# Kernel optimization log

Measured on AMD Instinct MI355X. Metric: run time of the kernel, lower is better.

## Reference

```python
import jax, jax.numpy as jnp
import numpy as np

K = 7  # kernel_size


def setup_inputs() -> dict:
    key = jax.random.key(0)
    k1, k2 = jax.random.split(key)
    kernels = jax.random.normal(k1, (4, K, K, 256, 256), dtype=jnp.float32)
    features = jax.random.normal(k2, (4, 96, 256, 256), dtype=jnp.float32)
    return {"kernels": kernels, "features": features}


def reference(kernels, features):
    # kernels: [b, k, k, h, w]; features: [b, c, h, w]
    # Equivalent to unfold(features) viewed as [b,c,k,k,h,w] contracted with
    # kernels via einsum 'bcklhw,bklhw->bchw', but computed as a fused sum of
    # k*k shifted products to avoid materializing the k^2-larger intermediate.
    b, c, h, w = features.shape
    k = kernels.shape[1]
    p = k // 2
    fpad = jnp.pad(features, ((0, 0), (0, 0), (p, p), (p, p)))
    out = jnp.zeros_like(features)
    for i in range(k):  # small fixed loop over kernel taps (k*k = 49)
        for j in range(k):
            out = out + fpad[:, :, i:i + h, j:j + w] * kernels[:, i, j][:, None]
    return out
```

## Files before the change

### kernel.cpp

```cpp
#include <hip/hip_runtime.h>


#define BATCH 4
#define CHAN 96
#define HH_ 256
#define WW_ 256
#define KS 7
#define PADR 3
#define TW 32
#define TH 16
#define CG 4
#define NCQ (CHAN / CG)
#define HALO_W (TW + KS - 1)
#define HALO_H (TH + KS - 1)
#define STAGE_N (HALO_H * HALO_W * CG)
#define NTHR 256
#define SPT ((STAGE_N + NTHR - 1) / NTHR)

__global__ __launch_bounds__(NTHR, 2)
void svconv_kernel(const float* __restrict__ kernels,
                   const float* __restrict__ features,
                   float* __restrict__ out) {
    __shared__ float lds[STAGE_N];

    const int tid = threadIdx.x;
    const int xt = blockIdx.x;
    const int yt = blockIdx.y;
    const int b  = blockIdx.z;

    const int tx  = tid & (TW - 1);
    const int yi  = tid >> 5;
    const int gx  = xt * TW + tx;
    const int ly0 = 2 * yi;
    const int gy0 = yt * TH + ly0;

    float kr[2][KS][KS];
#pragma unroll
    for (int s = 0; s < 2; ++s)
#pragma unroll
        for (int i = 0; i < KS; ++i)
#pragma unroll
            for (int j = 0; j < KS; ++j)
                kr[s][i][j] = kernels[((((size_t)b * KS + i) * KS + j) * HH_ + (gy0 + s)) * WW_ + gx];

    float rbuf[SPT];

    auto stage_load = [&](int cq) {
        const int c0 = cq * CG;
#pragma unroll
        for (int t = 0; t < SPT; ++t) {
            const int idx = tid + NTHR * t;
            float v = 0.0f;
            if (idx < STAGE_N) {
                const int c   = idx & (CG - 1);
                const int pix = idx >> 2;
                const int rx  = pix % HALO_W;
                const int ry  = pix / HALO_W;
                const int fy  = yt * TH + ry - PADR;
                const int fx  = xt * TW + rx - PADR;
                if ((unsigned)fy < (unsigned)HH_ && (unsigned)fx < (unsigned)WW_)
                    v = features[(((size_t)b * CHAN + (c0 + c)) * HH_ + fy) * WW_ + fx];
            }
            rbuf[t] = v;
        }
    };

    stage_load(0);

    for (int cq = 0; cq < NCQ; ++cq) {
        __syncthreads();
#pragma unroll
        for (int t = 0; t < SPT; ++t) {
            const int idx = tid + NTHR * t;
            if (idx < STAGE_N) lds[idx] = rbuf[t];
        }
        __syncthreads();

        if (cq + 1 < NCQ) stage_load(cq + 1);

        const float4* lds4 = reinterpret_cast<const float4*>(lds);

        float acc[2][CG];
#pragma unroll
        for (int s = 0; s < 2; ++s)
#pragma unroll
            for (int q = 0; q < CG; ++q) acc[s][q] = 0.0f;

#pragma unroll
        for (int roff = 0; roff < KS + 1; ++roff) {
            const int r = ly0 + roff;
            float4 w[KS];
#pragma unroll
            for (int rxo = 0; rxo < KS; ++rxo)
                w[rxo] = lds4[r * HALO_W + tx + rxo];
#pragma unroll
            for (int rxo = 0; rxo < KS; ++rxo) {
#pragma unroll
                for (int s = 0; s < 2; ++s) {
                    const int i = roff - s;
                    if (i >= 0 && i < KS) {
                        const float k = kr[s][i][rxo];
                        acc[s][0] += w[rxo].x * k;
                        acc[s][1] += w[rxo].y * k;
                        acc[s][2] += w[rxo].z * k;
                        acc[s][3] += w[rxo].w * k;
                    }
                }
            }
        }

        const int c0 = cq * CG;
#pragma unroll
        for (int s = 0; s < 2; ++s)
#pragma unroll
            for (int q = 0; q < CG; ++q)
                out[(((size_t)b * CHAN + (c0 + q)) * HH_ + (gy0 + s)) * WW_ + gx] = acc[s][q];
    }
}

extern "C" void kernel_launch(void* const* d_in, const int* in_sizes, int n_in,
                              void* d_out, int out_size, void* d_ws, size_t ws_size,
                              hipStream_t stream) {
    const float* kernels  = (const float*)d_in[0];
    const float* features = (const float*)d_in[1];
    float* out = (float*)d_out;

    dim3 grid(WW_ / TW, HH_ / TH, BATCH);
    dim3 block(NTHR);
    svconv_kernel<<<grid, block, 0, stream>>>(kernels, features, out);
}
```

Before: 75.25 us.

## Enlarge tile to 32x32 with four rows per thread and clamped halo loads

```diff
diff --git a/kernel.cpp b/kernel.cpp
--- a/kernel.cpp
+++ b/kernel.cpp
@@ -3,118 +3,120 @@
 
 #define BATCH 4
 #define CHAN 96
-#define HH_ 256
-#define WW_ 256
+#define HW_ 256
+#define HWPIX 65536
 #define KS 7
 #define PADR 3
 #define TW 32
-#define TH 16
+#define TH 32
+#define PXT 4
 #define CG 4
 #define NCQ (CHAN / CG)
-#define HALO_W (TW + KS - 1)
-#define HALO_H (TH + KS - 1)
-#define STAGE_N (HALO_H * HALO_W * CG)
+#define HALO 38
+#define PLANE (HALO * HALO)
+#define STAGE_DW (PLANE * CG)
 #define NTHR 256
-#define SPT ((STAGE_N + NTHR - 1) / NTHR)
+#define SPT 23
 
-__global__ __launch_bounds__(NTHR, 2)
-void svconv_kernel(const float* __restrict__ kernels,
-                   const float* __restrict__ features,
-                   float* __restrict__ out) {
-    __shared__ float lds[STAGE_N];
+__global__ __launch_bounds__(NTHR, 1)
+void svconv_kernel(const float* __restrict__ K_, const float* __restrict__ F_,
+                   float* __restrict__ O_) {
+    __shared__ float lds[STAGE_DW];
 
     const int tid = threadIdx.x;
-    const int xt = blockIdx.x;
-    const int yt = blockIdx.y;
-    const int b  = blockIdx.z;
+    const int xt = blockIdx.x, yt = blockIdx.y, b = blockIdx.z;
+    const int tx  = tid & 31;
+    const int ty  = tid >> 5;
+    const int gx  = xt * TW + tx;
+    const int gy0 = yt * TH + ty * PXT;
 
-    const int tx  = tid & (TW - 1);
-    const int yi  = tid >> 5;
-    const int gx  = xt * TW + tx;
-    const int ly0 = 2 * yi;
-    const int gy0 = yt * TH + ly0;
-
-    float kr[2][KS][KS];
+    float kr[PXT][KS][KS];
 #pragma unroll
-    for (int s = 0; s < 2; ++s)
+    for (int s = 0; s < PXT; ++s)
 #pragma unroll
         for (int i = 0; i < KS; ++i)
 #pragma unroll
-            for (int j = 0; j < KS; ++j)
-                kr[s][i][j] = kernels[((((size_t)b * KS + i) * KS + j) * HH_ + (gy0 + s)) * WW_ + gx];
+            for (int j = 0; j < KS; ++j) {
+                float v = K_[((((size_t)b * KS + i) * KS + j) * HW_ + (gy0 + s)) * HW_ + gx];
+                const int fy = gy0 + s + i - PADR;
+                const int fx = gx + j - PADR;
+                kr[s][i][j] = ((unsigned)fy < (unsigned)HW_ && (unsigned)fx < (unsigned)HW_) ? v : 0.0f;
+            }
+
+    unsigned voff[SPT];
+#pragma unroll
+    for (int t = 0; t < SPT; ++t) {
+        int idx = t * NTHR + tid;
+        if (idx >= STAGE_DW) idx = STAGE_DW - 1;
+        const int c  = idx & (CG - 1);
+        const int ps = idx >> 2;
+        const int ry = ps / HALO;
+        const int rx = ps - ry * HALO;
+        int fy = yt * TH + ry - PADR; fy = fy < 0 ? 0 : (fy > HW_ - 1 ? HW_ - 1 : fy);
+        int fx = xt * TW + rx - PADR; fx = fx < 0 ? 0 : (fx > HW_ - 1 ? HW_ - 1 : fx);
+        voff[t] = (unsigned)((c * HWPIX + fy * HW_ + fx) * 4);
+    }
+
+    const char* fb = (const char*)(F_ + (size_t)b * CHAN * HWPIX);
 
     float rbuf[SPT];
+#pragma unroll
+    for (int t = 0; t < SPT; ++t)
+        rbuf[t] = *(const float*)(fb + voff[t]);
 
-    auto stage_load = [&](int cq) {
-        const int c0 = cq * CG;
+#pragma unroll 1
+    for (int cq = 0; cq < NCQ; ++cq) {
 #pragma unroll
         for (int t = 0; t < SPT; ++t) {
-            const int idx = tid + NTHR * t;
-            float v = 0.0f;
-            if (idx < STAGE_N) {
-                const int c   = idx & (CG - 1);
-                const int pix = idx >> 2;
-                const int rx  = pix % HALO_W;
-                const int ry  = pix / HALO_W;
-                const int fy  = yt * TH + ry - PADR;
-                const int fx  = xt * TW + rx - PADR;
-                if ((unsigned)fy < (unsigned)HH_ && (unsigned)fx < (unsigned)WW_)
-                    v = features[(((size_t)b * CHAN + (c0 + c)) * HH_ + fy) * WW_ + fx];
-            }
-            rbuf[t] = v;
+            const int idx = t * NTHR + tid;
+            if (idx < STAGE_DW) lds[idx] = rbuf[t];
         }
-    };
 
-    stage_load(0);
+        if (cq + 1 < NCQ) {
+            const char* fb2 = fb + (size_t)(cq + 1) * CG * HWPIX * 4;
+#pragma unroll
+            for (int t = 0; t < SPT; ++t)
+                rbuf[t] = *(const float*)(fb2 + voff[t]);
+        }
 
-    for (int cq = 0; cq < NCQ; ++cq) {
-        __syncthreads();
-#pragma unroll
-        for (int t = 0; t < SPT; ++t) {
-            const int idx = tid + NTHR * t;
-            if (idx < STAGE_N) lds[idx] = rbuf[t];
-        }
         __syncthreads();
 
-        if (cq + 1 < NCQ) stage_load(cq + 1);
-
-        const float4* lds4 = reinterpret_cast<const float4*>(lds);
-
-        float acc[2][CG];
+        const float4* L = (const float4*)lds;
+        float acc[PXT][CG];
 #pragma unroll
-        for (int s = 0; s < 2; ++s)
+        for (int s = 0; s < PXT; ++s)
 #pragma unroll
             for (int q = 0; q < CG; ++q) acc[s][q] = 0.0f;
 
 #pragma unroll
-        for (int roff = 0; roff < KS + 1; ++roff) {
-            const int r = ly0 + roff;
-            float4 w[KS];
-#pragma unroll
-            for (int rxo = 0; rxo < KS; ++rxo)
-                w[rxo] = lds4[r * HALO_W + tx + rxo];
+        for (int roff = 0; roff < PXT + KS - 1; ++roff) {
+            const int rb = (ty * PXT + roff) * HALO + tx;
 #pragma unroll
             for (int rxo = 0; rxo < KS; ++rxo) {
+                const float4 w = L[rb + rxo];
 #pragma unroll
-                for (int s = 0; s < 2; ++s) {
+                for (int s = 0; s < PXT; ++s) {
                     const int i = roff - s;
                     if (i >= 0 && i < KS) {
                         const float k = kr[s][i][rxo];
-                        acc[s][0] += w[rxo].x * k;
-                        acc[s][1] += w[rxo].y * k;
-                        acc[s][2] += w[rxo].z * k;
-                        acc[s][3] += w[rxo].w * k;
+                        acc[s][0] += w.x * k;
+                        acc[s][1] += w.y * k;
+                        acc[s][2] += w.z * k;
+                        acc[s][3] += w.w * k;
                     }
                 }
             }
         }
 
-        const int c0 = cq * CG;
+        float* ob = O_ + (size_t)b * CHAN * HWPIX + (size_t)cq * CG * HWPIX
+                  + (size_t)gy0 * HW_ + gx;
 #pragma unroll
-        for (int s = 0; s < 2; ++s)
+        for (int q = 0; q < CG; ++q)
 #pragma unroll
-            for (int q = 0; q < CG; ++q)
-                out[(((size_t)b * CHAN + (c0 + q)) * HH_ + (gy0 + s)) * WW_ + gx] = acc[s][q];
+            for (int s = 0; s < PXT; ++s)
+                ob[(size_t)q * HWPIX + s * HW_] = acc[s][q];
+
+        __syncthreads();
     }
 }
 
@@ -125,7 +127,7 @@
     const float* features = (const float*)d_in[1];
     float* out = (float*)d_out;
 
-    dim3 grid(WW_ / TW, HH_ / TH, BATCH);
+    dim3 grid(HW_ / TW, HW_ / TH, BATCH);
     dim3 block(NTHR);
     svconv_kernel<<<grid, block, 0, stream>>>(kernels, features, out);
 }
```

After: 129.3 us. 1.72x slower.
